# Performance work log

Measured on AMD Instinct MI355X. Metric: run time of the kernel, lower is better.

The kernel has to match this reference:

```python
import jax, jax.numpy as jnp
import numpy as np

EPS = 1e-8
LAM = 1.0


def setup_inputs() -> dict:
    key = jax.random.key(0)
    k1, k2 = jax.random.split(key)
    B, H, W = 32, 512, 512
    output = jax.random.normal(k1, (B, 1, H, W), dtype=jnp.float32)
    target = jax.random.normal(k2, (B, 1, H, W), dtype=jnp.float32)
    return {"output": output, "target": target}


def _frc_loss(output, target):
    # squeeze channel dim: (B,1,H,W) -> (B,H,W)
    output = output[:, 0]
    target = target[:, 0]
    B, H, W = output.shape
    rnyquist = H // 2

    # radial index map (H,W): round(sqrt(fx^2 + fy^2)) in pixel-frequency units
    fx = jnp.fft.fftfreq(H, 1.0 / H)
    fy = jnp.fft.fftfreq(W, 1.0 / W)
    X, Y = jnp.meshgrid(fx, fy, indexing='ij')
    radial = jnp.round(jnp.sqrt(X ** 2 + Y ** 2)).astype(jnp.int32)
    # bins > rnyquist were ignored by the original loop -> dump into extra bin
    idx = jnp.where(radial > rnyquist, rnyquist + 1, radial).reshape(-1)  # (H*W,)

    F1 = jnp.fft.fft2(output, norm='forward')  # (B,H,W) complex
    F2 = jnp.fft.fft2(target, norm='forward')

    # per-pixel correlation terms, laid out (HW, B) for segment_sum over leading axis
    a = (F1.real * F2.real + F1.imag * F2.imag).reshape(B, -1).T
    b = (F1.imag * F2.real - F1.real * F2.imag).reshape(B, -1).T
    c1 = (F1.real ** 2 + F1.imag ** 2).reshape(B, -1).T
    c2 = (F2.real ** 2 + F2.imag ** 2).reshape(B, -1).T
    stacked = jnp.stack([a, b, c1, c2], axis=-1)  # (HW, B, 4)

    # single-pass radial-bin segment sum (replaces O(R*H*W) masked loop)
    sums = jax.ops.segment_sum(stacked, idx, num_segments=rnyquist + 2)
    sums = sums[:rnyquist + 1]  # drop overflow bin -> (rnyquist+1, B, 4)
    C_r, C_i, C1, C2 = sums[..., 0], sums[..., 1], sums[..., 2], sums[..., 3]

    frc = jnp.sqrt(C_r ** 2 + C_i ** 2) / (jnp.sqrt(C1 * C2) + EPS)
    return LAM * jnp.mean((1.0 - frc) ** 2)


def reference(output, target):
    return _frc_loss(output, target)
```

## Files before the change

### kernel.cpp

```cpp
#include <hip/hip_runtime.h>
#include <math.h>

#define NIMG 32
#define NB3  771
#define NSLICE (NIMG * 8)
#define PI_F 3.14159265358979323846f

__device__ __forceinline__ float2 cadd(float2 a, float2 b){ return make_float2(a.x+b.x, a.y+b.y); }
__device__ __forceinline__ float2 csub(float2 a, float2 b){ return make_float2(a.x-b.x, a.y-b.y); }
__device__ __forceinline__ float2 cmul(float2 a, float2 b){ return make_float2(a.x*b.x - a.y*b.y, a.x*b.y + a.y*b.x); }
__device__ __forceinline__ float2 cmul_mi(float2 a){ return make_float2(a.y, -a.x); }
__device__ __forceinline__ float2 tw(const float2* T, int m){ return T[m + (m >> 3)]; }
__device__ __forceinline__ int   sw(int pos){ return pos + (pos >> 3); }

__device__ __forceinline__ void dft8(float2* x) {
    const float c = 0.70710678118654752f;
    float2 u0 = cadd(x[0], x[4]), u1 = cadd(x[1], x[5]);
    float2 u2 = cadd(x[2], x[6]), u3 = cadd(x[3], x[7]);
    float2 v0 = csub(x[0], x[4]);
    float2 d1 = csub(x[1], x[5]);
    float2 v1 = make_float2(c*(d1.x + d1.y), c*(d1.y - d1.x));
    float2 d2 = csub(x[2], x[6]);
    float2 v2 = make_float2(d2.y, -d2.x);
    float2 d3 = csub(x[3], x[7]);
    float2 v3 = make_float2(-c*(d3.x - d3.y), -c*(d3.x + d3.y));
    float2 e0 = cadd(u0,u2), e1 = cadd(u1,u3);
    float2 f0 = csub(u0,u2), f1 = cmul_mi(csub(u1,u3));
    float2 g0 = cadd(v0,v2), g1 = cadd(v1,v3);
    float2 h0 = csub(v0,v2), h1 = cmul_mi(csub(v1,v3));
    x[0] = cadd(e0,e1); x[4] = csub(e0,e1);
    x[2] = cadd(f0,f1); x[6] = csub(f0,f1);
    x[1] = cadd(g0,g1); x[5] = csub(g0,g1);
    x[3] = cadd(h0,h1); x[7] = csub(h0,h1);
}

__device__ __forceinline__ void wave_fft512_dual(float2* Xa, float2* Xb,
                                                 float2* Sw, const float2* T,
                                                 int J) {
    dft8(Xa);
    dft8(Xb);
#pragma unroll
    for (int k = 1; k < 8; ++k) Xa[k] = cmul(Xa[k], tw(T, J * k));
#pragma unroll
    for (int k = 1; k < 8; ++k) Xb[k] = cmul(Xb[k], tw(T, J * k));
    const int jj = J + (J >> 3);
    const int j2 = J & 7;
    const int bb = 72 * (J >> 3) + j2;

#pragma unroll
    for (int k = 0; k < 8; ++k) Sw[jj + 72*k] = Xa[k];
#pragma unroll
    for (int q = 0; q < 8; ++q) Xa[q] = Sw[bb + 9*q];
#pragma unroll
    for (int k = 0; k < 8; ++k) Sw[jj + 72*k] = Xb[k];
#pragma unroll
    for (int q = 0; q < 8; ++q) Xb[q] = Sw[bb + 9*q];

    dft8(Xa);
    dft8(Xb);
#pragma unroll
    for (int k = 1; k < 8; ++k) Xa[k] = cmul(Xa[k], tw(T, 8 * j2 * k));
#pragma unroll
    for (int k = 1; k < 8; ++k) Xb[k] = cmul(Xb[k], tw(T, 8 * j2 * k));

#pragma unroll
    for (int k = 0; k < 8; ++k) Sw[bb + 9*k] = Xa[k];
#pragma unroll
    for (int q = 0; q < 8; ++q) Xa[q] = Sw[9*J + q];
#pragma unroll
    for (int k = 0; k < 8; ++k) Sw[bb + 9*k] = Xb[k];
#pragma unroll
    for (int q = 0; q < 8; ++q) Xb[q] = Sw[9*J + q];

    dft8(Xa);
    dft8(Xb);
}

__global__ __launch_bounds__(256) void fft_rows_T(const float* __restrict__ xr,
                                                  const float* __restrict__ yr,
                                                  float2* __restrict__ Zt,
                                                  float* __restrict__ sums,
                                                  unsigned int* __restrict__ counter) {
    __shared__ float2 S[4 * 576];
    __shared__ float2 T[576];
    const int t = threadIdx.x, w = t >> 6, J = t & 63;
    const int im = blockIdx.x >> 6, grp = blockIdx.x & 63;

    if (blockIdx.x < NSLICE) {
        float* z = sums + (size_t)blockIdx.x * NB3;
        for (int i = t; i < NB3; i += 256) z[i] = 0.0f;
        if (blockIdx.x == 0 && t == 0) *counter = 0u;
    }

#pragma unroll
    for (int i = 0; i < 2; ++i) {
        const int m = t + 256 * i;
        float s, c;
        __sincosf(-2.0f * PI_F * (float)m / 512.0f, &s, &c);
        T[m + (m >> 3)] = make_float2(c, s);
    }

    const size_t b0 = ((size_t)(im * 512 + grp * 8 + w)) << 9;
    const size_t b1 = b0 + (4u << 9);
    float2 X0[8], X1[8];
#pragma unroll
    for (int q = 0; q < 8; ++q) {
        X0[q] = make_float2(xr[b0 + J + 64*q], yr[b0 + J + 64*q]);
        X1[q] = make_float2(xr[b1 + J + 64*q], yr[b1 + J + 64*q]);
    }
    __syncthreads();

    float2* Sw = S + w * 576;
    wave_fft512_dual(X0, X1, Sw, T, J);

    const int r = ((J & 7) << 3) | (J >> 3);

#pragma unroll
    for (int k = 0; k < 8; ++k) Sw[64*k + r] = X0[k];
    __syncthreads();
    float2 eA[4], eB[4];
#pragma unroll
    for (int j = 0; j < 4; ++j) { eA[j] = S[j*576 + t]; eB[j] = S[j*576 + t + 256]; }
    __syncthreads();

#pragma unroll
    for (int k = 0; k < 8; ++k) Sw[64*k + r] = X1[k];
    __syncthreads();

    const size_t zb = ((size_t)im << 18) + ((size_t)grp << 12);
    {
        float4* o = (float4*)(Zt + zb + ((size_t)t << 3));
        float2 f0 = S[0*576 + t], f1 = S[1*576 + t];
        float2 f2 = S[2*576 + t], f3 = S[3*576 + t];
        o[0] = make_float4(eA[0].x, eA[0].y, eA[1].x, eA[1].y);
        o[1] = make_float4(eA[2].x, eA[2].y, eA[3].x, eA[3].y);
        o[2] = make_float4(f0.x, f0.y, f1.x, f1.y);
        o[3] = make_float4(f2.x, f2.y, f3.x, f3.y);
    }
    {
        float4* o = (float4*)(Zt + zb + ((size_t)(t + 256) << 3));
        float2 f0 = S[0*576 + t + 256], f1 = S[1*576 + t + 256];
        float2 f2 = S[2*576 + t + 256], f3 = S[3*576 + t + 256];
        o[0] = make_float4(eB[0].x, eB[0].y, eB[1].x, eB[1].y);
        o[1] = make_float4(eB[2].x, eB[2].y, eB[3].x, eB[3].y);
        o[2] = make_float4(f0.x, f0.y, f1.x, f1.y);
        o[3] = make_float4(f2.x, f2.y, f3.x, f3.y);
    }
}

__global__ __launch_bounds__(256) void fft_cols_rings(const float2* __restrict__ Zt,
                                                      float* __restrict__ sums,
                                                      unsigned int* __restrict__ counter,
                                                      float* __restrict__ out) {
    __shared__ float2 S[4 * 576];
    __shared__ float2 T[576];
    __shared__ float  bins[258 * 3];
    __shared__ int    lastFlag;
    const int t = threadIdx.x, w = t >> 6, J = t & 63;
    const int im = blockIdx.x >> 6, g = blockIdx.x & 63;
    const int p = 4 * g + w;

#pragma unroll
    for (int i = 0; i < 2; ++i) {
        const int m = t + 256 * i;
        float s, c;
        __sincosf(-2.0f * PI_F * (float)m / 512.0f, &s, &c);
        T[m + (m >> 3)] = make_float2(c, s);
    }
    for (int i = t; i < 258 * 3; i += 256) bins[i] = 0.0f;

    const int c0 = (p == 0) ? 0   : p;
    const int c1 = (p == 0) ? 256 : 512 - p;
    const size_t ibase = (size_t)im << 18;
    const int lane8 = J & 7, hi8 = J >> 3;
    const float2* q0 = Zt + ibase + ((size_t)c0 << 3) + lane8;
    const float2* q1 = Zt + ibase + ((size_t)c1 << 3) + lane8;
    float2 X0[8], X1[8];
#pragma unroll
    for (int q = 0; q < 8; ++q) {
        const size_t off = (size_t)(hi8 + 8*q) << 12;
        X0[q] = q0[off];
        X1[q] = q1[off];
    }
    __syncthreads();

    float2* A = S + w * 576;
    const int r  = ((J & 7) << 3) | (J >> 3);
    const int pk = r + (r >> 3);

    const float scale = 1.0f / (512.0f * 512.0f);
    auto pix = [&](float2 zk, float2 zm, float& av, float& c1v, float& c2v) {
        float f1r = 0.5f * (zk.x + zm.x) * scale;
        float f1i = 0.5f * (zk.y - zm.y) * scale;
        float f2r = 0.5f * (zk.y + zm.y) * scale;
        float f2i = 0.5f * (zm.x - zk.x) * scale;
        av  = f1r * f2r + f1i * f2i;
        c1v = f1r * f1r + f1i * f1i;
        c2v = f2r * f2r + f2i * f2i;
    };
    auto flush = [&](int ring, float a, float b, float c) {
        if (ring >= 0 && ring <= 256) {
            unsafeAtomicAdd(&bins[ring*3+0], a);
            unsafeAtomicAdd(&bins[ring*3+1], b);
            unsafeAtomicAdd(&bins[ring*3+2], c);
        }
    };

    wave_fft512_dual(X0, X1, A, T, J);

#pragma unroll
    for (int k = 0; k < 8; ++k) A[72*k + pk] = X0[k];

    float2 asv[8];
    if (p == 0) {
        int cur0 = -1;
        float a0 = 0, b0 = 0, c0v = 0;
#pragma unroll
        for (int i = 0; i < 8; ++i) {
            const int ky  = 8*J + i;
            const int kyp = (512 - ky) & 511;
            float2 zk = A[sw(ky)], zm = A[sw(kyp)];
            const float fk = (ky < 256) ? (float)ky : (float)(ky - 512);
            float av, cv, dv;
            pix(zk, zm, av, cv, dv);
            int rr = (int)rintf(fabsf(fk)); if (rr > 256) rr = 257;
            if (rr != cur0) { flush(cur0, a0, b0, c0v); cur0 = rr; a0 = av; b0 = cv; c0v = dv; }
            else            { a0 += av; b0 += cv; c0v += dv; }
        }
        flush(cur0, a0, b0, c0v);
    } else {
#pragma unroll
        for (int i = 0; i < 8; ++i) asv[i] = A[9*J + i];
    }

#pragma unroll
    for (int k = 0; k < 8; ++k) A[72*k + pk] = X1[k];

    if (p == 0) {
        int cur1 = -1;
        float a1 = 0, b1 = 0, c1v = 0;
#pragma unroll
        for (int i = 0; i < 8; ++i) {
            const int ky  = 8*J + i;
            const int kyp = (512 - ky) & 511;
            float2 zk = A[sw(ky)], zm = A[sw(kyp)];
            const float fk = (ky < 256) ? (float)ky : (float)(ky - 512);
            float av, cv, dv;
            pix(zk, zm, av, cv, dv);
            int rr = (int)rintf(sqrtf(fk*fk + 65536.0f)); if (rr > 256) rr = 257;
            if (rr != cur1) { flush(cur1, a1, b1, c1v); cur1 = rr; a1 = av; b1 = cv; c1v = dv; }
            else            { a1 += av; b1 += cv; c1v += dv; }
        }
        flush(cur1, a1, b1, c1v);
    } else {
        const float fy2 = (float)p * (float)p;
        int curR = -1;
        float sA = 0, sB = 0, sC = 0;
#pragma unroll
        for (int i = 0; i < 8; ++i) {
            const int ky  = 8*J + i;
            const int kyp = (512 - ky) & 511;
            float2 zk = asv[i];
            float2 zm = A[sw(kyp)];
            float a1v, b1v, d1v;
            pix(zk, zm, a1v, b1v, d1v);
            const float fk = (ky < 256) ? (float)ky : (float)(ky - 512);
            int rr = (int)rintf(sqrtf(fk*fk + fy2)); if (rr > 256) rr = 257;
            const float aa = 2.0f*a1v, bb = 2.0f*b1v, cc = 2.0f*d1v;
            if (rr != curR) { flush(curR, sA, sB, sC); curR = rr; sA = aa; sB = bb; sC = cc; }
            else            { sA += aa; sB += bb; sC += cc; }
        }
        flush(curR, sA, sB, sC);
    }
    __syncthreads();

    {
        float* dst = sums + (size_t)(im * 8 + (g & 7)) * NB3;
        for (int i = t; i < NB3; i += 256) unsafeAtomicAdd(&dst[i], bins[i]);
    }

    __syncthreads();
    if (t == 0) {
        __threadfence();
        unsigned int old = atomicAdd(counter, 1u);
        lastFlag = (old == (unsigned int)(gridDim.x - 1)) ? 1 : 0;
    }
    __syncthreads();
    if (lastFlag) {
        __threadfence();
        float acc = 0.0f;
        for (int idx = t; idx < NIMG * 257; idx += 256) {
            const int imQ = idx / 257;
            const int rr  = idx - imQ * 257;
            const float* pp = sums + (size_t)imQ * 8 * NB3 + rr * 3;
            float cr = 0.f, c1s = 0.f, c2s = 0.f;
#pragma unroll
            for (int s = 0; s < 8; ++s) {
                cr  += pp[(size_t)s * NB3 + 0];
                c1s += pp[(size_t)s * NB3 + 1];
                c2s += pp[(size_t)s * NB3 + 2];
            }
            float frc = fabsf(cr) / (sqrtf(c1s * c2s) + 1e-8f);
            float d = 1.0f - frc;
            acc += d * d;
        }
#pragma unroll
        for (int off = 32; off > 0; off >>= 1) acc += __shfl_down(acc, off);
        __shared__ float red[4];
        if ((t & 63) == 0) red[t >> 6] = acc;
        __syncthreads();
        if (t == 0)
            out[0] = (red[0] + red[1] + red[2] + red[3]) *
                     (1.0f / (257.0f * (float)NIMG));
    }
}

extern "C" void kernel_launch(void* const* d_in, const int* in_sizes, int n_in,
                              void* d_out, int out_size, void* d_ws, size_t ws_size,
                              hipStream_t stream) {
    const float* xr = (const float*)d_in[0];
    const float* yr = (const float*)d_in[1];

    float2* Zt = (float2*)d_ws;
    const size_t ztBytes = ((size_t)NIMG << 18) * sizeof(float2);
    float* sums = (float*)((char*)d_ws + ztBytes);
    unsigned int* counter = (unsigned int*)((char*)d_ws + ztBytes +
                              (size_t)NSLICE * NB3 * sizeof(float));

    fft_rows_T    <<<dim3(NIMG * 64), dim3(256), 0, stream>>>(xr, yr, Zt, sums, counter);
    fft_cols_rings<<<dim3(NIMG * 64), dim3(256), 0, stream>>>(Zt, sums, counter, (float*)d_out);
}
```

Before: 202.1 us.

## Store row-FFT output fully transposed so column kernel reads contiguous rows

The row-FFT kernel now runs 512-thread blocks that each transform 16 rows. Each thread writes 16 consecutive complex values into a plain transposed intermediate, replacing the earlier 8-wide tiled layout. The column kernel then reads each column as a contiguous 512-element row, so its global loads are fully coalesced instead of strided 64-byte chunks. In exchange, the row kernel's stores become 128-byte segments at a 4 KB stride between threads. It also uses more shared memory and fewer, larger blocks.

```diff
diff --git a/kernel.cpp b/kernel.cpp
--- a/kernel.cpp
+++ b/kernel.cpp
@@ -76,32 +76,30 @@
     dft8(Xb);
 }
 
-__global__ __launch_bounds__(256) void fft_rows_T(const float* __restrict__ xr,
+__global__ __launch_bounds__(512) void fft_rows_T(const float* __restrict__ xr,
                                                   const float* __restrict__ yr,
                                                   float2* __restrict__ Zt,
                                                   float* __restrict__ sums,
                                                   unsigned int* __restrict__ counter) {
-    __shared__ float2 S[4 * 576];
+    __shared__ float2 S[8 * 576];
     __shared__ float2 T[576];
     const int t = threadIdx.x, w = t >> 6, J = t & 63;
-    const int im = blockIdx.x >> 6, grp = blockIdx.x & 63;
+    const int im = blockIdx.x >> 5, grp = blockIdx.x & 31;
 
     if (blockIdx.x < NSLICE) {
         float* z = sums + (size_t)blockIdx.x * NB3;
-        for (int i = t; i < NB3; i += 256) z[i] = 0.0f;
+        for (int i = t; i < NB3; i += 512) z[i] = 0.0f;
         if (blockIdx.x == 0 && t == 0) *counter = 0u;
     }
 
-#pragma unroll
-    for (int i = 0; i < 2; ++i) {
-        const int m = t + 256 * i;
+    {
         float s, c;
-        __sincosf(-2.0f * PI_F * (float)m / 512.0f, &s, &c);
-        T[m + (m >> 3)] = make_float2(c, s);
-    }
-
-    const size_t b0 = ((size_t)(im * 512 + grp * 8 + w)) << 9;
-    const size_t b1 = b0 + (4u << 9);
+        __sincosf(-2.0f * PI_F * (float)t / 512.0f, &s, &c);
+        T[t + (t >> 3)] = make_float2(c, s);
+    }
+
+    const size_t b0 = ((size_t)(im * 512 + grp * 16 + w)) << 9;
+    const size_t b1 = b0 + ((size_t)8 << 9);
     float2 X0[8], X1[8];
 #pragma unroll
     for (int q = 0; q < 8; ++q) {
@@ -118,34 +116,28 @@
 #pragma unroll
     for (int k = 0; k < 8; ++k) Sw[64*k + r] = X0[k];
     __syncthreads();
-    float2 eA[4], eB[4];
-#pragma unroll
-    for (int j = 0; j < 4; ++j) { eA[j] = S[j*576 + t]; eB[j] = S[j*576 + t + 256]; }
+    float2 eA[8];
+#pragma unroll
+    for (int j = 0; j < 8; ++j) eA[j] = S[j*576 + t];
     __syncthreads();
 
 #pragma unroll
     for (int k = 0; k < 8; ++k) Sw[64*k + r] = X1[k];
     __syncthreads();
-
-    const size_t zb = ((size_t)im << 18) + ((size_t)grp << 12);
-    {
-        float4* o = (float4*)(Zt + zb + ((size_t)t << 3));
-        float2 f0 = S[0*576 + t], f1 = S[1*576 + t];
-        float2 f2 = S[2*576 + t], f3 = S[3*576 + t];
-        o[0] = make_float4(eA[0].x, eA[0].y, eA[1].x, eA[1].y);
-        o[1] = make_float4(eA[2].x, eA[2].y, eA[3].x, eA[3].y);
-        o[2] = make_float4(f0.x, f0.y, f1.x, f1.y);
-        o[3] = make_float4(f2.x, f2.y, f3.x, f3.y);
-    }
-    {
-        float4* o = (float4*)(Zt + zb + ((size_t)(t + 256) << 3));
-        float2 f0 = S[0*576 + t + 256], f1 = S[1*576 + t + 256];
-        float2 f2 = S[2*576 + t + 256], f3 = S[3*576 + t + 256];
-        o[0] = make_float4(eB[0].x, eB[0].y, eB[1].x, eB[1].y);
-        o[1] = make_float4(eB[2].x, eB[2].y, eB[3].x, eB[3].y);
-        o[2] = make_float4(f0.x, f0.y, f1.x, f1.y);
-        o[3] = make_float4(f2.x, f2.y, f3.x, f3.y);
-    }
+    float2 eB[8];
+#pragma unroll
+    for (int j = 0; j < 8; ++j) eB[j] = S[j*576 + t];
+
+    float4* o = (float4*)(Zt + ((size_t)im << 18) + ((size_t)t << 9)
+                             + (size_t)(grp * 16));
+    o[0] = make_float4(eA[0].x, eA[0].y, eA[1].x, eA[1].y);
+    o[1] = make_float4(eA[2].x, eA[2].y, eA[3].x, eA[3].y);
+    o[2] = make_float4(eA[4].x, eA[4].y, eA[5].x, eA[5].y);
+    o[3] = make_float4(eA[6].x, eA[6].y, eA[7].x, eA[7].y);
+    o[4] = make_float4(eB[0].x, eB[0].y, eB[1].x, eB[1].y);
+    o[5] = make_float4(eB[2].x, eB[2].y, eB[3].x, eB[3].y);
+    o[6] = make_float4(eB[4].x, eB[4].y, eB[5].x, eB[5].y);
+    o[7] = make_float4(eB[6].x, eB[6].y, eB[7].x, eB[7].y);
 }
 
 __global__ __launch_bounds__(256) void fft_cols_rings(const float2* __restrict__ Zt,
@@ -171,17 +163,11 @@
 
     const int c0 = (p == 0) ? 0   : p;
     const int c1 = (p == 0) ? 256 : 512 - p;
-    const size_t ibase = (size_t)im << 18;
-    const int lane8 = J & 7, hi8 = J >> 3;
-    const float2* q0 = Zt + ibase + ((size_t)c0 << 3) + lane8;
-    const float2* q1 = Zt + ibase + ((size_t)c1 << 3) + lane8;
+    const float2* rp0 = Zt + ((size_t)im << 18) + ((size_t)c0 << 9);
+    const float2* rp1 = Zt + ((size_t)im << 18) + ((size_t)c1 << 9);
     float2 X0[8], X1[8];
 #pragma unroll
-    for (int q = 0; q < 8; ++q) {
-        const size_t off = (size_t)(hi8 + 8*q) << 12;
-        X0[q] = q0[off];
-        X1[q] = q1[off];
-    }
+    for (int q = 0; q < 8; ++q) { X0[q] = rp0[J + 64*q]; X1[q] = rp1[J + 64*q]; }
     __syncthreads();
 
     float2* A = S + w * 576;
@@ -327,6 +313,6 @@
     unsigned int* counter = (unsigned int*)((char*)d_ws + ztBytes +
                               (size_t)NSLICE * NB3 * sizeof(float));
 
-    fft_rows_T    <<<dim3(NIMG * 64), dim3(256), 0, stream>>>(xr, yr, Zt, sums, counter);
+    fft_rows_T    <<<dim3(NIMG * 32), dim3(512), 0, stream>>>(xr, yr, Zt, sums, counter);
     fft_cols_rings<<<dim3(NIMG * 64), dim3(256), 0, stream>>>(Zt, sums, counter, (float*)d_out);
 }
```

Result: faster. 196.3 us (-2.9%).
